# Kernel tuning notes

Measured on AMD Instinct MI355X. Metric: run time of the kernel, lower is better.

The kernel has to match this reference:

```python
import jax, jax.numpy as jnp
import numpy as np

BN_EPS = 1e-5
# regular 3x3 kernel grid offsets: row0 = dy, row1 = dx, kernel positions in row-major order
REG = jnp.array([[-1, -1, -1, 0, 0, 0, 1, 1, 1],
                 [-1,  0,  1, -1, 0, 1, -1, 0, 1]], dtype=jnp.float32)


def conv3x3(x, w, b):
    y = jax.lax.conv_general_dilated(x, w, window_strides=(1, 1),
                                     padding=((1, 1), (1, 1)),
                                     dimension_numbers=('NCHW', 'OIHW', 'NCHW'))
    return y + b[None, :, None, None]


def deform_conv3x3(x, dy, dx, w):
    # x: [N,C,H,W]; dy,dx: [N,9,H,W] per-kernel-tap offsets; w: [O,C,3,3]
    N, C, H, W = x.shape
    K = 9
    ky = jnp.repeat(jnp.arange(3), 3)   # [0,0,0,1,1,1,2,2,2]
    kx = jnp.tile(jnp.arange(3), 3)     # [0,1,2,0,1,2,0,1,2]
    # sampling positions: p = p_out - pad + k*dilation + offset (stride=1, pad=dil=1)
    py = dy + (jnp.arange(H) - 1)[None, None, :, None] + ky[None, :, None, None].astype(x.dtype)
    px = dx + (jnp.arange(W) - 1)[None, None, None, :] + kx[None, :, None, None].astype(x.dtype)
    y0 = jnp.floor(py)
    x0 = jnp.floor(px)
    wy = py - y0  # bilinear weights
    wx = px - x0
    y0i = y0.astype(jnp.int32)
    x0i = x0.astype(jnp.int32)
    nidx = jnp.arange(N)[:, None, None, None]

    def gather(yi, xi):
        valid = ((yi >= 0) & (yi < H) & (xi >= 0) & (xi < W)).astype(x.dtype)
        v = x[nidx, :, jnp.clip(yi, 0, H - 1), jnp.clip(xi, 0, W - 1)]  # [N,K,H,W,C]
        return v * valid[..., None]

    sampled = (gather(y0i,     x0i)     * ((1 - wy) * (1 - wx))[..., None]
             + gather(y0i,     x0i + 1) * ((1 - wy) * wx)[..., None]
             + gather(y0i + 1, x0i)     * (wy * (1 - wx))[..., None]
             + gather(y0i + 1, x0i + 1) * (wy * wx)[..., None])  # [N,K,H,W,C]
    O = w.shape[0]
    return jnp.einsum('nkhwc,ock->nohw', sampled, w.reshape(O, C, K))


def setup_inputs() -> dict:
    key = jax.random.key(0)
    ks = jax.random.split(key, 12)
    N, C, H, W = 2, 256, 96, 96
    O = 256
    sc = 1.0 / np.sqrt(C * 9)
    return {
        'x': jax.random.normal(ks[0], (N, C, H, W), jnp.float32),
        'mask_attention': jax.random.normal(ks[1], (N, C, H, W), jnp.float32),
        'w_tm': jax.random.normal(ks[2], (4, C, 3, 3), jnp.float32) * sc,
        'b_tm': jax.random.normal(ks[3], (4,), jnp.float32) * 0.01,
        'w_tr': jax.random.normal(ks[4], (2, C, 3, 3), jnp.float32) * sc,
        'b_tr': jax.random.normal(ks[5], (2,), jnp.float32) * 0.01,
        'w_deform': jax.random.normal(ks[6], (O, C, 3, 3), jnp.float32) * sc,
        'bn_gamma': jnp.ones((O,), jnp.float32),
        'bn_beta': jnp.zeros((O,), jnp.float32),
        'bn_mean': jax.random.normal(ks[7], (O,), jnp.float32) * 0.01,
        'bn_var': jax.random.uniform(ks[8], (O,), jnp.float32, 0.5, 1.5),
    }


def reference(x, mask_attention, w_tm, b_tm, w_tr, b_tr, w_deform,
              bn_gamma, bn_beta, bn_mean, bn_var):
    # mask_attention is overwritten by x in the original forward; ignored.
    N, C, H, W = x.shape
    tm = conv3x3(x, w_tm, b_tm)                       # [N,4,H,W]
    T = tm.transpose(0, 2, 3, 1).reshape(N, H, W, 2, 2)
    off = jnp.einsum('nhwij,jk->nhwik', T, REG) - REG  # [N,H,W,2,9], (T-I)@REG
    tr = conv3x3(x, w_tr, b_tr)                        # [N,2,H,W]
    off = off + tr.transpose(0, 2, 3, 1)[..., None]    # broadcast translation to all 9 taps
    dy = off[..., 0, :].transpose(0, 3, 1, 2)          # [N,9,H,W]
    dx = off[..., 1, :].transpose(0, 3, 1, 2)
    out = deform_conv3x3(x, dy, dx, w_deform)          # [N,O,H,W]
    inv = jax.lax.rsqrt(bn_var + BN_EPS)
    out = (out - bn_mean[None, :, None, None]) * (inv * bn_gamma)[None, :, None, None] \
          + bn_beta[None, :, None, None]
    return jax.nn.relu(out + x)
```

## Files before the change

kernel.cpp:

```cpp
#include <hip/hip_runtime.h>
#include <stdint.h>

#define H_ 96
#define W_ 96
#define C_ 256
#define O_ 256
#define N_ 2
#define HW_ (H_*W_)
#define M_ (N_*HW_)
#define GK 2304

typedef __bf16 bf16x8 __attribute__((ext_vector_type(8)));
typedef float f32x4 __attribute__((ext_vector_type(4)));
typedef float f32x2 __attribute__((ext_vector_type(2)));
typedef unsigned short us4 __attribute__((ext_vector_type(4)));
typedef unsigned short us8 __attribute__((ext_vector_type(8)));

__device__ __forceinline__ unsigned short f2bf(float f) {
  union { float f; unsigned int u; } v; v.f = f;
  unsigned int u = v.u;
  return (unsigned short)((u + 0x7fffu + ((u >> 16) & 1u)) >> 16);
}
__device__ __forceinline__ float bf2f(unsigned short h) {
  union { unsigned int u; float f; } v; v.u = ((unsigned int)h) << 16;
  return v.f;
}
__device__ __forceinline__ f32x2 bfpair(unsigned int a) {
  union { unsigned int u; float f; } lo, hi;
  lo.u = a << 16;
  hi.u = a & 0xffff0000u;
  f32x2 r; r[0] = lo.f; r[1] = hi.f;
  return r;
}

__global__ __launch_bounds__(256) void k_pre(const float* __restrict__ x,
                                             const float* __restrict__ w_df,
                                             const float* __restrict__ w_tm,
                                             const float* __restrict__ w_tr,
                                             unsigned short* __restrict__ xt,
                                             unsigned short* __restrict__ wfrag,
                                             unsigned short* __restrict__ w6p) {
  const int b = blockIdx.x;
  const int tid = threadIdx.x;
  if (b < 576) {
    __shared__ unsigned short tile[64][130];
    const int pt = b % 144;
    const int ch = (b / 144) & 1;
    const int n  = b / 288;
    const int p0 = pt * 64, c0 = ch * 128;
    const float* xp = x + (size_t)n * C_ * HW_;
    unsigned short* xtp = xt + (size_t)n * C_ * HW_;
    const int tx = tid & 15, ty = tid >> 4;
#pragma unroll
    for (int pass = 0; pass < 8; pass++) {
      const int c = pass * 16 + ty;
      const f32x4 v = *(const f32x4*)(xp + (size_t)(c0 + c) * HW_ + p0 + tx * 4);
#pragma unroll
      for (int i = 0; i < 4; i++) tile[tx * 4 + i][c] = f2bf(v[i]);
    }
    __syncthreads();
    const int l32 = tid & 31, pr = tid >> 5;
#pragma unroll
    for (int pass = 0; pass < 8; pass++) {
      const int p = pass * 8 + pr;
      us4 v;
#pragma unroll
      for (int i = 0; i < 4; i++) v[i] = tile[p][l32 * 4 + i];
      *(us4*)(xtp + (size_t)(p0 + p) * C_ + c0 + l32 * 4) = v;
    }
  } else if (b < 864) {
    const int base = (b - 576) * 2048 + tid * 8;
    const int l  = (base >> 3) & 63;
    const int g  = (base >> 9) & 15;
    const int ks = (base >> 13) & 7;
    const int t  = base >> 16;
    const int o  = g * 16 + (l & 15);
    const int c  = ks * 32 + (l >> 4) * 8;
    us8 res;
#pragma unroll
    for (int j = 0; j < 8; j++) res[j] = f2bf(w_df[(size_t)(o * 256 + c + j) * 9 + t]);
    *(us8*)(wfrag + base) = res;
  } else {
    int idx = (b - 864) * 256 + tid;
    int t = idx >> 12;
    int r = idx & 4095;
    int j = r >> 8;
    int c = r & 255;
    float v = 0.f;
    if (j < 4) v = w_tm[(size_t)(j * C_ + c) * 9 + t];
    else if (j < 6) v = w_tr[(size_t)((j - 4) * C_ + c) * 9 + t];
    w6p[idx] = f2bf(v);
  }
}

__global__ __launch_bounds__(512, 4) void k_fused(const unsigned short* __restrict__ xt,
                                                  const unsigned short* __restrict__ Wfrag,
                                                  const unsigned short* __restrict__ w6p,
                                                  const float* __restrict__ b_tm,
                                                  const float* __restrict__ b_tr,
                                                  const float* __restrict__ xres,
                                                  const float* __restrict__ gamma,
                                                  const float* __restrict__ beta,
                                                  const float* __restrict__ mean,
                                                  const float* __restrict__ var,
                                                  float* __restrict__ out) {
  __shared__ unsigned short As[2][32 * 256] __attribute__((aligned(16)));
  __shared__ float sred[8][16][8];
  __shared__ float coords_s[32][9][2];
  const int tid = threadIdx.x;
  const int wave = tid >> 6, lane = tid & 63;
  const int row = lane & 15, quad = lane >> 4;
  const int slot = (blockIdx.x & 7) * 144 + (blockIdx.x >> 3);
  const int bm = slot >> 1;
  const int bo = slot & 1;
  const int m0 = bm * 32;
  const int n = m0 / HW_;
  const int sr = tid >> 4;
  const int cg = tid & 15;

  {
    const int hw0 = m0 - n * HW_;
    const int h = hw0 / W_;
    const int w0 = hw0 - h * W_;
    const int rh = wave >> 2;
    const int cq = (wave & 3) * 64;
    f32x4 oacc = {0.f, 0.f, 0.f, 0.f};
    const bf16x8 zero8 = {};
#pragma unroll
    for (int t = 0; t < 9; t++) {
      const int ty = t / 3, tx = t % 3;
      const int y = h + ty - 1;
      if (y < 0 || y >= H_) continue;
      const int xx = w0 + rh * 16 + row + tx - 1;
      const bool valid = (xx >= 0) && (xx < W_);
      const int xc = min(max(xx, 0), W_ - 1);
      const unsigned short* arow =
          xt + (size_t)((n * H_ + y) * W_ + xc) * C_ + cq + quad * 8;
      const unsigned short* brow =
          w6p + (size_t)(t * 16 + row) * C_ + cq + quad * 8;
#pragma unroll
      for (int ks = 0; ks < 2; ks++) {
        bf16x8 av = *(const bf16x8*)(const void*)(arow + ks * 32);
        if (!valid) av = zero8;
        bf16x8 bv = *(const bf16x8*)(const void*)(brow + ks * 32);
        oacc = __builtin_amdgcn_mfma_f32_16x16x32_bf16(av, bv, oacc, 0, 0, 0);
      }
    }
    if (row < 6) {
#pragma unroll
      for (int r = 0; r < 4; r++) sred[wave][quad * 4 + r][row] = oacc[r];
    }
  }
  __syncthreads();
  if (wave < 2 && lane < 16) {
    const int rg = wave * 16 + lane;
    const int hwm = m0 + rg - n * HW_;
    const int h = hwm / W_, w = hwm - h * W_;
    float a[6];
#pragma unroll
    for (int j = 0; j < 6; j++)
      a[j] = sred[wave * 4 + 0][lane][j] + sred[wave * 4 + 1][lane][j] +
             sred[wave * 4 + 2][lane][j] + sred[wave * 4 + 3][lane][j];
    const float tm0 = a[0] + b_tm[0];
    const float tm1 = a[1] + b_tm[1];
    const float tm2 = a[2] + b_tm[2];
    const float tm3 = a[3] + b_tm[3];
    const float tr0 = a[4] + b_tr[0];
    const float tr1 = a[5] + b_tr[1];
#pragma unroll
    for (int t = 0; t < 9; t++) {
      const float ry = (float)(t / 3) - 1.f;
      const float rx = (float)(t % 3) - 1.f;
      coords_s[rg][t][0] = (float)h + tr0 + tm0 * ry + tm1 * rx;
      coords_s[rg][t][1] = (float)w + tr1 + tm2 * ry + tm3 * rx;
    }
  }
  __syncthreads();

  f32x4 acc0 = {}, acc1 = {};
  float cw[4];
  int cb[4];
  us8 u0[4], u1[4];

#define PREP1(TAP)                                                             \
  {                                                                            \
    const float py = coords_s[sr][TAP][0];                                     \
    const float px = coords_s[sr][TAP][1];                                     \
    const float fy = floorf(py), fx = floorf(px);                              \
    const float wy = py - fy, wx = px - fx;                                    \
    const int y0 = (int)fy, x0 = (int)fx;                                      \
    const int y1 = y0 + 1, x1 = x0 + 1;                                        \
    const float vy0 = (y0 >= 0 && y0 < H_) ? 1.f : 0.f;                        \
    const float vy1 = (y1 >= 0 && y1 < H_) ? 1.f : 0.f;                        \
    const float vx0 = (x0 >= 0 && x0 < W_) ? 1.f : 0.f;                        \
    const float vx1 = (x1 >= 0 && x1 < W_) ? 1.f : 0.f;                        \
    cw[0] = (1.f - wy) * (1.f - wx) * vy0 * vx0;                               \
    cw[1] = (1.f - wy) * wx * vy0 * vx1;                                       \
    cw[2] = wy * (1.f - wx) * vy1 * vx0;                                       \
    cw[3] = wy * wx * vy1 * vx1;                                               \
    const int cy0 = min(max(y0, 0), H_ - 1), cy1 = min(max(y1, 0), H_ - 1);    \
    const int cx0 = min(max(x0, 0), W_ - 1), cx1 = min(max(x1, 0), W_ - 1);    \
    cb[0] = ((n * H_ + cy0) * W_ + cx0) * C_;                                  \
    cb[1] = ((n * H_ + cy0) * W_ + cx1) * C_;                                  \
    cb[2] = ((n * H_ + cy1) * W_ + cx0) * C_;                                  \
    cb[3] = ((n * H_ + cy1) * W_ + cx1) * C_;                                  \
  }

#define LOADC1()                                                               \
  {                                                                            \
    const int cc = cg * 16;                                                    \
    u0[0] = *(const us8*)(xt + cb[0] + cc); u1[0] = *(const us8*)(xt + cb[0] + cc + 8); \
    u0[1] = *(const us8*)(xt + cb[1] + cc); u1[1] = *(const us8*)(xt + cb[1] + cc + 8); \
    u0[2] = *(const us8*)(xt + cb[2] + cc); u1[2] = *(const us8*)(xt + cb[2] + cc + 8); \
    u0[3] = *(const us8*)(xt + cb[3] + cc); u1[3] = *(const us8*)(xt + cb[3] + cc + 8); \
  }

#define LERP8V(DST, U)                                                         \
  {                                                                            \
    const unsigned int* a0 = (const unsigned int*)&U[0];                       \
    const unsigned int* a1 = (const unsigned int*)&U[1];                       \
    const unsigned int* a2 = (const unsigned int*)&U[2];                       \
    const unsigned int* a3 = (const unsigned int*)&U[3];                       \
    _Pragma("unroll")                                                          \
    for (int p = 0; p < 4; p++) {                                              \
      f32x2 acc = bfpair(a0[p]) * cw[0] + bfpair(a1[p]) * cw[1] +              \
                  bfpair(a2[p]) * cw[2] + bfpair(a3[p]) * cw[3];               \
      DST[p * 2]     = (__bf16)acc[0];                                         \
      DST[p * 2 + 1] = (__bf16)acc[1];                                         \
    }                                                                          \
  }

  PREP1(0);
  LOADC1();

  for (int tap = 0; tap < 9; tap++) {
    unsigned short* __restrict__ asb = As[tap & 1];

    const unsigned short* wfTap =
        Wfrag + (size_t)tap * 65536 + (bo * 8 + wave) * 512 + lane * 8;
    bf16x8 bv = *(const bf16x8*)(const void*)(wfTap);

    {
      const int q0 = cg * 2, q1 = cg * 2 + 1;
      const int s0 = (q0 & 24) | ((q0 ^ sr) & 7);
      const int s1 = (q1 & 24) | ((q1 ^ sr) & 7);
      bf16x8 r0, r1;
      LERP8V(r0, u0);
      LERP8V(r1, u1);
      *(bf16x8*)(void*)&asb[sr * 256 + s0 * 8] = r0;
      *(bf16x8*)(void*)&asb[sr * 256 + s1 * 8] = r1;
    }

    __syncthreads();

    if (tap < 8) {
      PREP1(tap + 1);
      LOADC1();
    }

#pragma unroll
    for (int ks = 0; ks < 8; ks++) {
      const int q = ks * 4 + quad;
      const int slot = (q & 24) | ((q ^ row) & 7);
      const bf16x8 av0 = *(const bf16x8*)(const void*)&asb[row * 256 + slot * 8];
      const bf16x8 av1 = *(const bf16x8*)(const void*)&asb[(row + 16) * 256 + slot * 8];
      bf16x8 bn;
      if (ks < 7) bn = *(const bf16x8*)(const void*)(wfTap + (size_t)(ks + 1) * 8192);
      acc0 = __builtin_amdgcn_mfma_f32_16x16x32_bf16(av0, bv, acc0, 0, 0, 0);
      acc1 = __builtin_amdgcn_mfma_f32_16x16x32_bf16(av1, bv, acc1, 0, 0, 0);
      if (ks < 7) bv = bn;
    }
  }

  const int hwb = m0 - n * HW_ + quad * 4;
  {
    const int o = bo * 128 + wave * 16 + row;
    const float sc = rsqrtf(var[o] + 1e-5f) * gamma[o];
    const float bi = beta[o] - mean[o] * sc;
    const size_t ob0 = (size_t)(n * O_ + o) * HW_ + hwb;
    f32x4 rv = *(const f32x4*)(xres + ob0);
    f32x4 ov;
#pragma unroll
    for (int r = 0; r < 4; r++) ov[r] = fmaxf(acc0[r] * sc + bi + rv[r], 0.f);
    *(f32x4*)(out + ob0) = ov;
    const size_t ob1 = ob0 + 16;
    rv = *(const f32x4*)(xres + ob1);
#pragma unroll
    for (int r = 0; r < 4; r++) ov[r] = fmaxf(acc1[r] * sc + bi + rv[r], 0.f);
    *(f32x4*)(out + ob1) = ov;
  }
}

extern "C" void kernel_launch(void* const* d_in, const int* in_sizes, int n_in,
                              void* d_out, int out_size, void* d_ws, size_t ws_size,
                              hipStream_t stream) {
  const float* x     = (const float*)d_in[0];
  const float* w_tm  = (const float*)d_in[2];
  const float* b_tm  = (const float*)d_in[3];
  const float* w_tr  = (const float*)d_in[4];
  const float* b_tr  = (const float*)d_in[5];
  const float* w_df  = (const float*)d_in[6];
  const float* gamma = (const float*)d_in[7];
  const float* beta  = (const float*)d_in[8];
  const float* mean  = (const float*)d_in[9];
  const float* var   = (const float*)d_in[10];
  float* out = (float*)d_out;

  char* ws = (char*)d_ws;
  unsigned short* xt    = (unsigned short*)(ws);
  unsigned short* wfrag = (unsigned short*)(ws + 9437184);
  unsigned short* w6p   = (unsigned short*)(ws + 9437184 + 1179648);

  k_pre<<<1008, 256, 0, stream>>>(x, w_df, w_tm, w_tr, xt, wfrag, w6p);
  k_fused<<<1152, 512, 0, stream>>>(xt, wfrag, w6p, b_tm, b_tr, x,
                                    gamma, beta, mean, var, out);
}
```

Before: 193.4 us.

## Switch to fp16 with packed-half bilinear lerp and cover all 256 outputs per block

```diff
diff --git a/kernel.cpp b/kernel.cpp
--- a/kernel.cpp
+++ b/kernel.cpp
@@ -10,27 +10,16 @@
 #define M_ (N_*HW_)
 #define GK 2304
 
-typedef __bf16 bf16x8 __attribute__((ext_vector_type(8)));
+typedef _Float16 f16x8 __attribute__((ext_vector_type(8)));
+typedef _Float16 f16x2 __attribute__((ext_vector_type(2)));
 typedef float f32x4 __attribute__((ext_vector_type(4)));
-typedef float f32x2 __attribute__((ext_vector_type(2)));
 typedef unsigned short us4 __attribute__((ext_vector_type(4)));
 typedef unsigned short us8 __attribute__((ext_vector_type(8)));
 
-__device__ __forceinline__ unsigned short f2bf(float f) {
-  union { float f; unsigned int u; } v; v.f = f;
-  unsigned int u = v.u;
-  return (unsigned short)((u + 0x7fffu + ((u >> 16) & 1u)) >> 16);
-}
-__device__ __forceinline__ float bf2f(unsigned short h) {
-  union { unsigned int u; float f; } v; v.u = ((unsigned int)h) << 16;
-  return v.f;
-}
-__device__ __forceinline__ f32x2 bfpair(unsigned int a) {
-  union { unsigned int u; float f; } lo, hi;
-  lo.u = a << 16;
-  hi.u = a & 0xffff0000u;
-  f32x2 r; r[0] = lo.f; r[1] = hi.f;
-  return r;
+__device__ __forceinline__ unsigned short f2h(float f) {
+  union { _Float16 h; unsigned short u; } v;
+  v.h = (_Float16)f;
+  return v.u;
 }
 
 __global__ __launch_bounds__(256) void k_pre(const float* __restrict__ x,
@@ -56,7 +45,7 @@
       const int c = pass * 16 + ty;
       const f32x4 v = *(const f32x4*)(xp + (size_t)(c0 + c) * HW_ + p0 + tx * 4);
 #pragma unroll
-      for (int i = 0; i < 4; i++) tile[tx * 4 + i][c] = f2bf(v[i]);
+      for (int i = 0; i < 4; i++) tile[tx * 4 + i][c] = f2h(v[i]);
     }
     __syncthreads();
     const int l32 = tid & 31, pr = tid >> 5;
@@ -78,7 +67,7 @@
     const int c  = ks * 32 + (l >> 4) * 8;
     us8 res;
 #pragma unroll
-    for (int j = 0; j < 8; j++) res[j] = f2bf(w_df[(size_t)(o * 256 + c + j) * 9 + t]);
+    for (int j = 0; j < 8; j++) res[j] = f2h(w_df[(size_t)(o * 256 + c + j) * 9 + t]);
     *(us8*)(wfrag + base) = res;
   } else {
     int idx = (b - 864) * 256 + tid;
@@ -89,11 +78,11 @@
     float v = 0.f;
     if (j < 4) v = w_tm[(size_t)(j * C_ + c) * 9 + t];
     else if (j < 6) v = w_tr[(size_t)((j - 4) * C_ + c) * 9 + t];
-    w6p[idx] = f2bf(v);
+    w6p[idx] = f2h(v);
   }
 }
 
-__global__ __launch_bounds__(512, 4) void k_fused(const unsigned short* __restrict__ xt,
+__global__ __launch_bounds__(512, 3) void k_fused(const unsigned short* __restrict__ xt,
                                                   const unsigned short* __restrict__ Wfrag,
                                                   const unsigned short* __restrict__ w6p,
                                                   const float* __restrict__ b_tm,
@@ -110,9 +99,7 @@
   const int tid = threadIdx.x;
   const int wave = tid >> 6, lane = tid & 63;
   const int row = lane & 15, quad = lane >> 4;
-  const int slot = (blockIdx.x & 7) * 144 + (blockIdx.x >> 3);
-  const int bm = slot >> 1;
-  const int bo = slot & 1;
+  const int bm = (blockIdx.x & 7) * 72 + (blockIdx.x >> 3);
   const int m0 = bm * 32;
   const int n = m0 / HW_;
   const int sr = tid >> 4;
@@ -125,7 +112,7 @@
     const int rh = wave >> 2;
     const int cq = (wave & 3) * 64;
     f32x4 oacc = {0.f, 0.f, 0.f, 0.f};
-    const bf16x8 zero8 = {};
+    const f16x8 zero8 = {};
 #pragma unroll
     for (int t = 0; t < 9; t++) {
       const int ty = t / 3, tx = t % 3;
@@ -140,10 +127,10 @@
           w6p + (size_t)(t * 16 + row) * C_ + cq + quad * 8;
 #pragma unroll
       for (int ks = 0; ks < 2; ks++) {
-        bf16x8 av = *(const bf16x8*)(const void*)(arow + ks * 32);
+        f16x8 av = *(const f16x8*)(const void*)(arow + ks * 32);
         if (!valid) av = zero8;
-        bf16x8 bv = *(const bf16x8*)(const void*)(brow + ks * 32);
-        oacc = __builtin_amdgcn_mfma_f32_16x16x32_bf16(av, bv, oacc, 0, 0, 0);
+        f16x8 bv = *(const f16x8*)(const void*)(brow + ks * 32);
+        oacc = __builtin_amdgcn_mfma_f32_16x16x32_f16(av, bv, oacc, 0, 0, 0);
       }
     }
     if (row < 6) {
@@ -177,8 +164,8 @@
   }
   __syncthreads();
 
-  f32x4 acc0 = {}, acc1 = {};
-  float cw[4];
+  f32x4 acc0[2] = {}, acc1[2] = {};
+  f16x2 cwh0, cwh1, cwh2, cwh3;
   int cb[4];
   us8 u0[4], u1[4];
 
@@ -194,10 +181,14 @@
     const float vy1 = (y1 >= 0 && y1 < H_) ? 1.f : 0.f;                        \
     const float vx0 = (x0 >= 0 && x0 < W_) ? 1.f : 0.f;                        \
     const float vx1 = (x1 >= 0 && x1 < W_) ? 1.f : 0.f;                        \
-    cw[0] = (1.f - wy) * (1.f - wx) * vy0 * vx0;                               \
-    cw[1] = (1.f - wy) * wx * vy0 * vx1;                                       \
-    cw[2] = wy * (1.f - wx) * vy1 * vx0;                                       \
-    cw[3] = wy * wx * vy1 * vx1;                                               \
+    const float c0f = (1.f - wy) * (1.f - wx) * vy0 * vx0;                     \
+    const float c1f = (1.f - wy) * wx * vy0 * vx1;                             \
+    const float c2f = wy * (1.f - wx) * vy1 * vx0;                             \
+    const float c3f = wy * wx * vy1 * vx1;                                     \
+    const _Float16 h0 = (_Float16)c0f, h1 = (_Float16)c1f;                     \
+    const _Float16 h2 = (_Float16)c2f, h3 = (_Float16)c3f;                     \
+    cwh0 = (f16x2){h0, h0}; cwh1 = (f16x2){h1, h1};                            \
+    cwh2 = (f16x2){h2, h2}; cwh3 = (f16x2){h3, h3};                            \
     const int cy0 = min(max(y0, 0), H_ - 1), cy1 = min(max(y1, 0), H_ - 1);    \
     const int cx0 = min(max(x0, 0), W_ - 1), cx1 = min(max(x1, 0), W_ - 1);    \
     cb[0] = ((n * H_ + cy0) * W_ + cx0) * C_;                                  \
@@ -217,16 +208,18 @@
 
 #define LERP8V(DST, U)                                                         \
   {                                                                            \
-    const unsigned int* a0 = (const unsigned int*)&U[0];                       \
-    const unsigned int* a1 = (const unsigned int*)&U[1];                       \
-    const unsigned int* a2 = (const unsigned int*)&U[2];                       \
-    const unsigned int* a3 = (const unsigned int*)&U[3];                       \
+    const f16x2* p0 = (const f16x2*)&U[0];                                     \
+    const f16x2* p1 = (const f16x2*)&U[1];                                     \
+    const f16x2* p2 = (const f16x2*)&U[2];                                     \
+    const f16x2* p3 = (const f16x2*)&U[3];                                     \
+    f16x2* d = (f16x2*)&DST;                                                   \
     _Pragma("unroll")                                                          \
     for (int p = 0; p < 4; p++) {                                              \
-      f32x2 acc = bfpair(a0[p]) * cw[0] + bfpair(a1[p]) * cw[1] +              \
-                  bfpair(a2[p]) * cw[2] + bfpair(a3[p]) * cw[3];               \
-      DST[p * 2]     = (__bf16)acc[0];                                         \
-      DST[p * 2 + 1] = (__bf16)acc[1];                                         \
+      f16x2 r = p0[p] * cwh0;                                                  \
+      r = p1[p] * cwh1 + r;                                                    \
+      r = p2[p] * cwh2 + r;                                                    \
+      r = p3[p] * cwh3 + r;                                                    \
+      d[p] = r;                                                                \
     }                                                                          \
   }
 
@@ -237,18 +230,20 @@
     unsigned short* __restrict__ asb = As[tap & 1];
 
     const unsigned short* wfTap =
-        Wfrag + (size_t)tap * 65536 + (bo * 8 + wave) * 512 + lane * 8;
-    bf16x8 bv = *(const bf16x8*)(const void*)(wfTap);
+        Wfrag + (size_t)(tap * 8) * 8192 + wave * 1024 + lane * 8;
+    f16x8 bv[2];
+#pragma unroll
+    for (int ot = 0; ot < 2; ot++) bv[ot] = *(const f16x8*)(const void*)(wfTap + ot * 512);
 
     {
       const int q0 = cg * 2, q1 = cg * 2 + 1;
       const int s0 = (q0 & 24) | ((q0 ^ sr) & 7);
       const int s1 = (q1 & 24) | ((q1 ^ sr) & 7);
-      bf16x8 r0, r1;
+      us8 r0, r1;
       LERP8V(r0, u0);
       LERP8V(r1, u1);
-      *(bf16x8*)(void*)&asb[sr * 256 + s0 * 8] = r0;
-      *(bf16x8*)(void*)&asb[sr * 256 + s1 * 8] = r1;
+      *(us8*)(void*)&asb[sr * 256 + s0 * 8] = r0;
+      *(us8*)(void*)&asb[sr * 256 + s1 * 8] = r1;
     }
 
     __syncthreads();
@@ -262,31 +257,43 @@
     for (int ks = 0; ks < 8; ks++) {
       const int q = ks * 4 + quad;
       const int slot = (q & 24) | ((q ^ row) & 7);
-      const bf16x8 av0 = *(const bf16x8*)(const void*)&asb[row * 256 + slot * 8];
-      const bf16x8 av1 = *(const bf16x8*)(const void*)&asb[(row + 16) * 256 + slot * 8];
-      bf16x8 bn;
-      if (ks < 7) bn = *(const bf16x8*)(const void*)(wfTap + (size_t)(ks + 1) * 8192);
-      acc0 = __builtin_amdgcn_mfma_f32_16x16x32_bf16(av0, bv, acc0, 0, 0, 0);
-      acc1 = __builtin_amdgcn_mfma_f32_16x16x32_bf16(av1, bv, acc1, 0, 0, 0);
-      if (ks < 7) bv = bn;
+      const f16x8 av0 = *(const f16x8*)(const void*)&asb[row * 256 + slot * 8];
+      const f16x8 av1 = *(const f16x8*)(const void*)&asb[(row + 16) * 256 + slot * 8];
+      f16x8 bn[2];
+      if (ks < 7) {
+        const unsigned short* wfn = wfTap + (size_t)(ks + 1) * 8192;
+#pragma unroll
+        for (int ot = 0; ot < 2; ot++) bn[ot] = *(const f16x8*)(const void*)(wfn + ot * 512);
+      }
+#pragma unroll
+      for (int ot = 0; ot < 2; ot++)
+        acc0[ot] = __builtin_amdgcn_mfma_f32_16x16x32_f16(av0, bv[ot], acc0[ot], 0, 0, 0);
+#pragma unroll
+      for (int ot = 0; ot < 2; ot++)
+        acc1[ot] = __builtin_amdgcn_mfma_f32_16x16x32_f16(av1, bv[ot], acc1[ot], 0, 0, 0);
+      if (ks < 7) {
+#pragma unroll
+        for (int ot = 0; ot < 2; ot++) bv[ot] = bn[ot];
+      }
     }
   }
 
   const int hwb = m0 - n * HW_ + quad * 4;
-  {
-    const int o = bo * 128 + wave * 16 + row;
+#pragma unroll
+  for (int ot = 0; ot < 2; ot++) {
+    const int o = wave * 32 + ot * 16 + row;
     const float sc = rsqrtf(var[o] + 1e-5f) * gamma[o];
     const float bi = beta[o] - mean[o] * sc;
     const size_t ob0 = (size_t)(n * O_ + o) * HW_ + hwb;
     f32x4 rv = *(const f32x4*)(xres + ob0);
     f32x4 ov;
 #pragma unroll
-    for (int r = 0; r < 4; r++) ov[r] = fmaxf(acc0[r] * sc + bi + rv[r], 0.f);
+    for (int r = 0; r < 4; r++) ov[r] = fmaxf(acc0[ot][r] * sc + bi + rv[r], 0.f);
     *(f32x4*)(out + ob0) = ov;
     const size_t ob1 = ob0 + 16;
     rv = *(const f32x4*)(xres + ob1);
 #pragma unroll
-    for (int r = 0; r < 4; r++) ov[r] = fmaxf(acc1[r] * sc + bi + rv[r], 0.f);
+    for (int r = 0; r < 4; r++) ov[r] = fmaxf(acc1[ot][r] * sc + bi + rv[r], 0.f);
     *(f32x4*)(out + ob1) = ov;
   }
 }
@@ -312,6 +319,6 @@
   unsigned short* w6p   = (unsigned short*)(ws + 9437184 + 1179648);
 
   k_pre<<<1008, 256, 0, stream>>>(x, w_df, w_tm, w_tr, xt, wfrag, w6p);
-  k_fused<<<1152, 512, 0, stream>>>(xt, wfrag, w6p, b_tm, b_tr, x,
-                                    gamma, beta, mean, var, out);
+  k_fused<<<576, 512, 0, stream>>>(xt, wfrag, w6p, b_tm, b_tr, x,
+                                   gamma, beta, mean, var, out);
 }
```

After: 184.2 us. 1.05x faster.
